# Kernel tuning notes

Hardware: AMD Instinct MI355X
Metric: run time of the kernel (lower is better)

## Reference

```python
import jax, jax.numpy as jnp
import numpy as np
from functools import partial

DN = ('NCHW', 'OIHW', 'NCHW')

def _conv(x, w, b, stride, pad):
    y = jax.lax.conv_general_dilated(x, w, (stride, stride), [(pad, pad), (pad, pad)], dimension_numbers=DN)
    return y + b[None, :, None, None]

def _leaky(x, s):
    return jnp.where(x >= 0, x, s * x)

def _lstm_gates(pre, c):
    # PyTorch gate order: i, f, g, o
    i, f, g, o = jnp.split(pre, 4, axis=-1)
    c_new = jax.nn.sigmoid(f) * c + jax.nn.sigmoid(i) * jnp.tanh(g)
    h_new = jax.nn.sigmoid(o) * jnp.tanh(c_new)
    return h_new, c_new

def setup_inputs() -> dict:
    key = jax.random.key(0)
    ks = iter(jax.random.split(key, 32))
    s = 0.05
    d = {}
    d['x'] = jax.random.normal(next(ks), (128, 3, 64, 64), jnp.float32)
    # conv stack params
    d['w1'] = jax.random.normal(next(ks), (64, 3, 7, 7)) * s;   d['b1'] = jnp.zeros((64,))
    d['w2'] = jax.random.normal(next(ks), (128, 64, 7, 7)) * s; d['b2'] = jnp.zeros((128,))
    d['w3'] = jax.random.normal(next(ks), (256, 128, 5, 5)) * s; d['b3'] = jnp.zeros((256,))
    d['w4'] = jax.random.normal(next(ks), (512, 256, 5, 5)) * s; d['b4'] = jnp.zeros((512,))
    d['w5'] = jax.random.normal(next(ks), (512, 512, 5, 5)) * s; d['b5'] = jnp.zeros((512,))
    # 2-layer LSTM (hidden=512), PyTorch layout: W_ih [4H, In], W_hh [4H, H]
    H = 512
    for l in range(2):
        d[f'wih{l}'] = jax.random.normal(next(ks), (4 * H, H)) * s
        d[f'whh{l}'] = jax.random.normal(next(ks), (4 * H, H)) * s
        d[f'bih{l}'] = jnp.zeros((4 * H,))
        d[f'bhh{l}'] = jnp.zeros((4 * H,))
    # FC head
    d['fw1'] = jax.random.normal(next(ks), (512, 512)) * s; d['fb1'] = jnp.zeros((512,))
    d['fw2'] = jax.random.normal(next(ks), (13, 512)) * s;  d['fb2'] = jnp.zeros((13,))
    return d

TIMESTEPS = 20

def reference(x, w1, b1, w2, b2, w3, b3, w4, b4, w5, b5,
              wih0, whh0, bih0, bhh0, wih1, whh1, bih1, bhh1,
              fw1, fb1, fw2, fb2):
    B = x.shape[0]
    h = _conv(x, w1, b1, 2, 3); h = _leaky(h, 0.2)
    h = _conv(h, w2, b2, 2, 0); h = _leaky(h, 0.2)
    h = _conv(h, w3, b3, 1, 0); h = _leaky(h, 0.2)
    h = _conv(h, w4, b4, 1, 0); h = _leaky(h, 0.2)
    h = _conv(h, w5, b5, 1, 0); h = _leaky(h, 0.2)
    feat = h.reshape(B, -1)  # [B, 512]
    H = 512
    # input to layer-0 is constant across timesteps: precompute Wx once
    xW0 = feat @ wih0.T + bih0 + bhh0  # [B, 4H]
    zeros = jnp.zeros((B, H), feat.dtype)

    def step(carry, _):
        h0, c0, h1, c1 = carry
        h0n, c0n = _lstm_gates(xW0 + h0 @ whh0.T, c0)
        pre1 = h0n @ wih1.T + bih1 + bhh1 + h1 @ whh1.T
        h1n, c1n = _lstm_gates(pre1, c1)
        return (h0n, c0n, h1n, c1n), h1n

    _, ys = jax.lax.scan(step, (zeros, zeros, zeros, zeros), None, length=TIMESTEPS)
    y = ys.reshape(TIMESTEPS * B, H)
    y = _leaky(y @ fw1.T + fb1, 0.01)
    y = jax.nn.sigmoid(y @ fw2.T + fb2)
    return y
```

## Files before the change

kernel.cpp:

```cpp
#include <hip/hip_runtime.h>
#include <math.h>

typedef _Float16 half_t;
typedef __attribute__((ext_vector_type(8))) _Float16 f16x8;
typedef __attribute__((ext_vector_type(4))) _Float16 f16x4;
typedef __attribute__((ext_vector_type(4))) float f32x4;

#define LEAKY(v, s) ((v) >= 0.f ? (v) : (s) * (v))

__device__ __forceinline__ float sig_(float x) { return 1.f / (1.f + expf(-x)); }
__device__ __forceinline__ half_t f2h(float f) { return (half_t)f; }

#define GLD(gp, lp)                                              \
  __builtin_amdgcn_global_load_lds(                              \
      (const __attribute__((address_space(1))) void*)(gp),       \
      (__attribute__((address_space(3))) void*)(lp), 16, 0, 0)

#define PHASE_WAIT(N)                                            \
  asm volatile("s_waitcnt vmcnt(" #N ")" ::: "memory");          \
  __builtin_amdgcn_s_barrier();                                  \
  __builtin_amdgcn_sched_barrier(0)

#define QOFF0 2048LL
#define QOFF1 4096LL
#define QOFF2 135168LL
#define QOFF3 266240LL
#define QOFF4 5283840LL
#define QOFF5 5310464LL
#define QOFF6 6359040LL
#define QOFF7 6621184LL
#define QOFF8 7669760LL
#define QOFF9 9766912LL

__global__ void prep_all(
    const float* __restrict__ x, const float* __restrict__ w1,
    const float* __restrict__ wih0, const float* __restrict__ whh0,
    const float* __restrict__ bih0, const float* __restrict__ bhh0,
    const float* __restrict__ wih1, const float* __restrict__ whh1,
    const float* __restrict__ bih1, const float* __restrict__ bhh1,
    const float* __restrict__ fw1,
    float* __restrict__ bg0, float* __restrict__ bg1,
    float* __restrict__ czero, unsigned* __restrict__ hzero,
    half_t* __restrict__ xpad, half_t* __restrict__ w1r,
    half_t* __restrict__ wih0h, half_t* __restrict__ fw1h,
    half_t* __restrict__ wcat0h, half_t* __restrict__ wcat1h) {
  long long i = (long long)blockIdx.x * blockDim.x + threadIdx.x;
  if (i < QOFF0) {
    bg0[i] = bih0[i] + bhh0[i];
  } else if (i < QOFF1) {
    long long j = i - QOFF0;
    bg1[j] = bih1[j] + bhh1[j];
  } else if (i < QOFF2) {
    czero[i - QOFF1] = 0.f;
  } else if (i < QOFF3) {
    hzero[i - QOFF2] = 0u;
  } else if (i < QOFF4) {
    long long j = i - QOFF3;
    int c = j & 7;
    long long t = j >> 3;
    int iw = t % 70; t /= 70;
    int ih = t % 70;
    int n = t / 70;
    float v = 0.f;
    if (c < 3 && ih >= 3 && ih < 67 && iw >= 3 && iw < 67)
      v = x[((n * 3 + c) * 64 + (ih - 3)) * 64 + (iw - 3)];
    xpad[j] = f2h(v);
  } else if (i < QOFF5) {
    int j = (int)(i - QOFF4);
    int kg = j % 416, co = j / 416;
    int ci = kg & 7, tap = kg >> 3;
    float v = 0.f;
    if (tap < 49 && ci < 3) {
      int kh = tap / 7, kw = tap % 7;
      v = w1[((co * 3 + ci) * 7 + kh) * 7 + kw];
    }
    w1r[j] = f2h(v);
  } else if (i < QOFF6) {
    int j = (int)(i - QOFF5);
    wih0h[j] = f2h(wih0[j]);
  } else if (i < QOFF7) {
    int j = (int)(i - QOFF6);
    fw1h[j] = f2h(fw1[j]);
  } else if (i < QOFF8) {
    int j = (int)(i - QOFF7);
    int r = j >> 9, k = j & 511;
    int u = r >> 2, g = r & 3;
    wcat0h[j] = f2h(whh0[(g * 512 + u) * 512 + k]);
  } else if (i < QOFF9) {
    int j = (int)(i - QOFF8);
    int r = j >> 10, k = j & 1023;
    int u = r >> 2, g = r & 3;
    int row = g * 512 + u;
    wcat1h[j] = f2h(k < 512 ? wih1[row * 512 + k] : whh1[row * 512 + (k - 512)]);
  }
}

__global__ __launch_bounds__(256) void prep_wT(
    const float* __restrict__ w2, const float* __restrict__ w3,
    const float* __restrict__ w4, const float* __restrict__ w5,
    half_t* __restrict__ w2r, half_t* __restrict__ w3r,
    half_t* __restrict__ w4r, half_t* __restrict__ w5r) {
  __shared__ float T[12800];
  int bid = blockIdx.x, tid = threadIdx.x;
  const float* W;
  half_t* D;
  int co, Cin, TAP, lg2;
  if (bid < 128) {
    W = w2; D = w2r; co = bid; Cin = 64; TAP = 49; lg2 = 6;
  } else if (bid < 384) {
    W = w3; D = w3r; co = bid - 128; Cin = 128; TAP = 25; lg2 = 7;
  } else if (bid < 896) {
    W = w4; D = w4r; co = bid - 384; Cin = 256; TAP = 25; lg2 = 8;
  } else {
    W = w5; D = w5r; co = bid - 896; Cin = 512; TAP = 25; lg2 = 9;
  }
  int n = Cin * TAP;
  const float* src = W + (size_t)co * n;
  for (int i = tid; i < n; i += 256) T[i] = src[i];
  __syncthreads();
  half_t* dst = D + (size_t)co * n;
  for (int j = tid; j < n; j += 256) {
    int ci = j & (Cin - 1);
    int tap = j >> lg2;
    dst[j] = f2h(T[ci * TAP + tap]);
  }
}

template <int KW, int S, int LOG2CIN, int OUTMODE>
__global__ __launch_bounds__(256) void conv_mfma(
    const half_t* __restrict__ xin, const half_t* __restrict__ wr,
    const float* __restrict__ bias, void* __restrict__ outp,
    int Hin, int Win, int Hout, int Wout, int Cout, int K, int ktiles, float slope,
    long long zstride) {
  constexpr int CIN = 1 << LOG2CIN;
  __shared__ half_t lds[4][4096];
  const int tid = threadIdx.x;
  const int lane = tid & 63, wid = tid >> 6;
  const int sRow = tid >> 2, sCh = tid & 3;
  const int sSwz = sCh ^ ((sRow ^ (sRow >> 2)) & 3);
  const int kt0 = blockIdx.z * ktiles;
  const half_t* gArow = wr + (size_t)(blockIdx.y * 64 + sRow) * K + sSwz * 8;
  int p = blockIdx.x * 64 + sRow;
  int hw = Hout * Wout;
  int n = p / hw;
  int rem = p - n * hw;
  int oh = rem / Wout;
  int ow = rem - oh * Wout;
  const half_t* xb = xin + ((size_t)(n * Hin + oh * S) * Win + ow * S) * CIN;
  const int fr = lane & 15, fc = lane >> 4;
  const int r0 = (wid & 1) * 32, c0 = (wid >> 1) * 32;
  const int sw = (fc ^ ((fr ^ (fr >> 2)) & 3)) * 8;
  const int ia0 = (r0 + fr) * 32 + sw;
  const int ia1 = (r0 + 16 + fr) * 32 + sw;
  const int ib0 = 2048 + (c0 + fr) * 32 + sw;
  const int ib1 = 2048 + (c0 + 16 + fr) * 32 + sw;

  auto stage = [&](int t, int buf) {
    GLD(gArow + (size_t)(kt0 + t) * 32, &lds[buf][wid * 512]);
    int kg = (kt0 + t) * 32 + sSwz * 8;
    int ci = kg & (CIN - 1);
    int tap = kg >> LOG2CIN;
    int kh = tap / KW, kw = tap - kh * KW;
    GLD(xb + (kh * Win + kw) * CIN + ci, &lds[buf][2048 + wid * 512]);
  };

  f32x4 acc00 = {0.f, 0.f, 0.f, 0.f};
  f32x4 acc01 = acc00, acc10 = acc00, acc11 = acc00;

  auto compute = [&](int buf) {
    const half_t* L = &lds[buf][0];
    f16x8 a0 = *(const f16x8*)&L[ia0];
    f16x8 a1 = *(const f16x8*)&L[ia1];
    f16x8 b0 = *(const f16x8*)&L[ib0];
    f16x8 b1 = *(const f16x8*)&L[ib1];
    acc00 = __builtin_amdgcn_mfma_f32_16x16x32_f16(a0, b0, acc00, 0, 0, 0);
    acc01 = __builtin_amdgcn_mfma_f32_16x16x32_f16(a0, b1, acc01, 0, 0, 0);
    acc10 = __builtin_amdgcn_mfma_f32_16x16x32_f16(a1, b0, acc10, 0, 0, 0);
    acc11 = __builtin_amdgcn_mfma_f32_16x16x32_f16(a1, b1, acc11, 0, 0, 0);
  };

  stage(0, 0);
  stage(1, 1);
  stage(2, 2);
  int t = 0;
  for (; t < ktiles - 3; ++t) {
    PHASE_WAIT(4);
    stage(t + 3, (t + 3) & 3);
    compute(t & 3);
  }
  PHASE_WAIT(4);
  compute(t & 3);
  ++t;
  PHASE_WAIT(2);
  compute(t & 3);
  ++t;
  PHASE_WAIT(0);
  compute(t & 3);

#pragma unroll
  for (int am = 0; am < 2; ++am) {
#pragma unroll
    for (int bn = 0; bn < 2; ++bn) {
      f32x4 a = am == 0 ? (bn == 0 ? acc00 : acc01) : (bn == 0 ? acc10 : acc11);
      int co = blockIdx.y * 64 + r0 + am * 16 + fc * 4;
      int px = blockIdx.x * 64 + c0 + bn * 16 + fr;
      size_t o = (size_t)px * Cout + co;
      if (OUTMODE == 2) {
        float* pb = (float*)outp + (size_t)blockIdx.z * zstride;
        *(f32x4*)&pb[o] = a;
      } else {
        f32x4 bb = *(const f32x4*)&bias[co];
        f32x4 v;
#pragma unroll
        for (int j = 0; j < 4; ++j) {
          float tt = a[j] + bb[j];
          v[j] = LEAKY(tt, slope);
        }
        if (OUTMODE == 1) {
          *(f32x4*)&((float*)outp)[o] = v;
        } else {
          f16x4 hv;
#pragma unroll
          for (int j = 0; j < 4; ++j) hv[j] = f2h(v[j]);
          *(f16x4*)&((half_t*)outp)[o] = hv;
        }
      }
    }
  }
}

template <int KW, int S, int LOG2CIN, int OUTMODE>
__global__ __launch_bounds__(256) void conv_mfma128(
    const half_t* __restrict__ xin, const half_t* __restrict__ wr,
    const float* __restrict__ bias, void* __restrict__ outp,
    int Hin, int Win, int Hout, int Wout, int Cout, int K, int ktiles, float slope,
    long long zstride, int Y, int G) {
  constexpr int CIN = 1 << LOG2CIN;
  __shared__ half_t lds[4][8192];
  const int L = blockIdx.x;
  const int bx = L / G;
  const int g = L % G;
  const int by = g % Y;
  const int bz = g / Y;
  const int tid = threadIdx.x;
  const int lane = tid & 63, wid = tid >> 6;
  const int sRow = tid >> 2, sCh = tid & 3;
  const int sSwz = sCh ^ ((sRow ^ (sRow >> 2)) & 3);
  const int kt0 = bz * ktiles;
  const half_t* gA0 = wr + (size_t)(by * 128 + sRow) * K + sSwz * 8;
  const half_t* gA1 = wr + (size_t)(by * 128 + 64 + sRow) * K + sSwz * 8;
  int hw = Hout * Wout;
  int p0 = bx * 128 + sRow;
  int n0 = p0 / hw, r0p = p0 - n0 * hw, oh0 = r0p / Wout, ow0 = r0p - oh0 * Wout;
  const half_t* xb0 = xin + ((size_t)(n0 * Hin + oh0 * S) * Win + ow0 * S) * CIN;
  int p1 = p0 + 64;
  int n1 = p1 / hw, r1p = p1 - n1 * hw, oh1 = r1p / Wout, ow1 = r1p - oh1 * Wout;
  const half_t* xb1 = xin + ((size_t)(n1 * Hin + oh1 * S) * Win + ow1 * S) * CIN;

  const int fr = lane & 15, fc = lane >> 4;
  const int wr_ = wid & 1, wc_ = wid >> 1;
  const int sw = (fc ^ ((fr ^ (fr >> 2)) & 3)) * 8;
  const int iaB = (wr_ * 64 + fr) * 32 + sw;
  const int ibB = 4096 + (wc_ * 64 + fr) * 32 + sw;

  auto stage = [&](int t, int buf) {
    half_t* LB = &lds[buf][0];
    GLD(gA0 + (size_t)(kt0 + t) * 32, LB + wid * 512);
    GLD(gA1 + (size_t)(kt0 + t) * 32, LB + 2048 + wid * 512);
    int kg = (kt0 + t) * 32 + sSwz * 8;
    int ci = kg & (CIN - 1);
    int tap = kg >> LOG2CIN;
    int kh = tap / KW, kw = tap - kh * KW;
    int xoff = (kh * Win + kw) * CIN + ci;
    GLD(xb0 + xoff, LB + 4096 + wid * 512);
    GLD(xb1 + xoff, LB + 6144 + wid * 512);
  };

  f32x4 acc[4][4];
#pragma unroll
  for (int i = 0; i < 4; ++i)
#pragma unroll
    for (int j = 0; j < 4; ++j) acc[i][j] = (f32x4){0.f, 0.f, 0.f, 0.f};

  auto compute = [&](int buf) {
    const half_t* L2 = &lds[buf][0];
    f16x8 a[4], b[4];
#pragma unroll
    for (int fi = 0; fi < 4; ++fi) a[fi] = *(const f16x8*)&L2[iaB + fi * 512];
#pragma unroll
    for (int fj = 0; fj < 4; ++fj) b[fj] = *(const f16x8*)&L2[ibB + fj * 512];
#pragma unroll
    for (int fi = 0; fi < 4; ++fi)
#pragma unroll
      for (int fj = 0; fj < 4; ++fj)
        acc[fi][fj] = __builtin_amdgcn_mfma_f32_16x16x32_f16(a[fi], b[fj], acc[fi][fj], 0, 0, 0);
  };

  stage(0, 0);
  stage(1, 1);
  stage(2, 2);
  int t = 0;
  for (; t < ktiles - 3; ++t) {
    PHASE_WAIT(8);
    stage(t + 3, (t + 3) & 3);
    compute(t & 3);
  }
  PHASE_WAIT(8);
  compute(t & 3);
  ++t;
  PHASE_WAIT(4);
  compute(t & 3);
  ++t;
  PHASE_WAIT(0);
  compute(t & 3);

#pragma unroll
  for (int fi = 0; fi < 4; ++fi) {
#pragma unroll
    for (int fj = 0; fj < 4; ++fj) {
      int co = by * 128 + wr_ * 64 + fi * 16 + fc * 4;
      int px = bx * 128 + wc_ * 64 + fj * 16 + fr;
      size_t o = (size_t)px * Cout + co;
      if (OUTMODE == 3) {
        half_t* pb = (half_t*)outp + (size_t)bz * zstride;
        f16x4 hv;
#pragma unroll
        for (int j = 0; j < 4; ++j) hv[j] = f2h(acc[fi][fj][j]);
        *(f16x4*)&pb[o] = hv;
      } else {
        f32x4 bb = *(const f32x4*)&bias[co];
        f16x4 hv;
#pragma unroll
        for (int j = 0; j < 4; ++j) {
          float tt = acc[fi][fj][j] + bb[j];
          hv[j] = f2h(LEAKY(tt, slope));
        }
        *(f16x4*)&((half_t*)outp)[o] = hv;
      }
    }
  }
}

__global__ void finalize_part(const float* __restrict__ pb, const float* __restrict__ bias,
                              half_t* __restrict__ out, int size, int nz) {
  int i = blockIdx.x * blockDim.x + threadIdx.x;
  if (i >= size) return;
  float s = bias[i & 511];
  for (int z = 0; z < nz; ++z) s += pb[(size_t)z * size + i];
  out[i] = f2h(LEAKY(s, 0.2f));
}

__global__ void finalize_h(const half_t* __restrict__ pb, const float* __restrict__ bias,
                           half_t* __restrict__ out, int size8, int nz, int cmask,
                           long long zstride) {
  int idx = blockIdx.x * blockDim.x + threadIdx.x;
  if (idx >= size8) return;
  long long i = (long long)idx * 8;
  float s[8];
#pragma unroll
  for (int q = 0; q < 8; ++q) s[q] = bias[(int)((i + q) & cmask)];
  for (int z = 0; z < nz; ++z) {
    f16x8 v = *(const f16x8*)&pb[(size_t)z * zstride + i];
#pragma unroll
    for (int q = 0; q < 8; ++q) s[q] += (float)v[q];
  }
  f16x8 o;
#pragma unroll
  for (int q = 0; q < 8; ++q) o[q] = f2h(LEAKY(s[q], 0.2f));
  *(f16x8*)&out[i] = o;
}

__global__ __launch_bounds__(256) void lstm_fused(
    const half_t* __restrict__ h0in, half_t* __restrict__ h0out,
    const half_t* __restrict__ h1in, half_t* __restrict__ h1out,
    const half_t* __restrict__ wcat0, const half_t* __restrict__ wcat1,
    const float* __restrict__ xw0, const float* __restrict__ bg1,
    float* __restrict__ c0, float* __restrict__ c1,
    half_t* __restrict__ ysout, int roles) {
  const bool isL1 = (roles == 2) || (blockIdx.z == 1);
  const int NT = isL1 ? 16 : 8;
  const half_t* wcat = isL1 ? wcat1 : wcat0;
  float* c = isL1 ? c1 : c0;
  half_t* hout = isL1 ? h1out : h0out;
  const int K = NT * 64;

  __shared__ half_t lds[4][8192];
  const int tid = threadIdx.x;
  const int lane = tid & 63, wid = tid >> 6;
  const int ybase = blockIdx.y * 64, bbase = blockIdx.x * 64;
  const int rA0 = wid * 16 + (lane >> 3);
  const int rA1 = rA0 + 8;
  const int chS = ((lane & 7) ^ ((lane >> 3) & 7)) * 8;
  const half_t* gA0 = wcat + (size_t)(ybase + rA0) * K + chS;
  const half_t* gA1 = wcat + (size_t)(ybase + rA1) * K + chS;
  const size_t hb0 = (size_t)(bbase + rA0) * 512 + chS;
  const size_t hb1 = (size_t)(bbase + rA1) * 512 + chS;

  auto stage = [&](int t, int buf) {
    GLD(gA0 + t * 64, &lds[buf][wid * 1024]);
    GLD(gA1 + t * 64, &lds[buf][wid * 1024 + 512]);
    const half_t* hs = (isL1 && t >= 8) ? h1in : h0in;
    int koff = (isL1 && t >= 8) ? (t - 8) * 64 : t * 64;
    GLD(hs + hb0 + koff, &lds[buf][4096 + wid * 1024]);
    GLD(hs + hb1 + koff, &lds[buf][4096 + wid * 1024 + 512]);
  };

  const int fr = lane & 15, fc = lane >> 4;
  const int wr_ = wid & 1, wc_ = wid >> 1;

  f32x4 acc[2][2];
#pragma unroll
  for (int fi = 0; fi < 2; ++fi)
#pragma unroll
    for (int fj = 0; fj < 2; ++fj) acc[fi][fj] = (f32x4){0.f, 0.f, 0.f, 0.f};

  auto compute = [&](int buf) {
    const half_t* L = &lds[buf][0];
#pragma unroll
    for (int s = 0; s < 2; ++s) {
      f16x8 a[2], b[2];
#pragma unroll
      for (int fi = 0; fi < 2; ++fi) {
        int row = wr_ * 32 + fi * 16 + fr;
        a[fi] = *(const f16x8*)&L[row * 64 + (((s * 4 + fc) ^ (fr & 7)) * 8)];
      }
#pragma unroll
      for (int fj = 0; fj < 2; ++fj) {
        int brow = wc_ * 32 + fj * 16 + fr;
        b[fj] = *(const f16x8*)&L[4096 + brow * 64 + (((s * 4 + fc) ^ (fr & 7)) * 8)];
      }
#pragma unroll
      for (int fi = 0; fi < 2; ++fi)
#pragma unroll
        for (int fj = 0; fj < 2; ++fj)
          acc[fi][fj] = __builtin_amdgcn_mfma_f32_16x16x32_f16(a[fi], b[fj], acc[fi][fj], 0, 0, 0);
    }
  };

  stage(0, 0);
  stage(1, 1);
  stage(2, 2);
  int t = 0;
  for (; t < NT - 3; ++t) {
    PHASE_WAIT(8);
    stage(t + 3, (t + 3) & 3);
    compute(t & 3);
  }
  PHASE_WAIT(8);
  compute(t & 3);
  ++t;
  PHASE_WAIT(4);
  compute(t & 3);
  ++t;
  PHASE_WAIT(0);
  compute(t & 3);

#pragma unroll
  for (int fi = 0; fi < 2; ++fi) {
#pragma unroll
    for (int fj = 0; fj < 2; ++fj) {
      int Rb = ybase + wr_ * 32 + fi * 16 + fc * 4;
      int u = Rb >> 2;
      int b = bbase + wc_ * 32 + fj * 16 + fr;
      float p[4];
#pragma unroll
      for (int j = 0; j < 4; ++j) {
        float s = acc[fi][fj][j];
        s += isL1 ? bg1[j * 512 + u] : xw0[b * 2048 + j * 512 + u];
        p[j] = s;
      }
      int ci = b * 512 + u;
      float cprev = c[ci];
      float ig = sig_(p[0]);
      float fg = sig_(p[1]);
      float gg = tanhf(p[2]);
      float og = sig_(p[3]);
      float cn = fg * cprev + ig * gg;
      float hn = og * tanhf(cn);
      c[ci] = cn;
      hout[ci] = f2h(hn);
      if (isL1) ysout[ci] = f2h(hn);
    }
  }
}

__global__ void fc2_sigmoid(const half_t* __restrict__ in, const float* __restrict__ w,
                            const float* __restrict__ b, float* __restrict__ out) {
  int idx = blockIdx.x * blockDim.x + threadIdx.x;
  if (idx >= 2560 * 13) return;
  int j = idx % 13, r = idx / 13;
  const half_t* ip = in + (size_t)r * 512;
  const float* wp = w + j * 512;
  float s = b[j];
  for (int k = 0; k < 512; k += 8) {
    f16x8 hv = *(const f16x8*)&ip[k];
#pragma unroll
    for (int q = 0; q < 8; ++q) s = fmaf((float)hv[q], wp[k + q], s);
  }
  out[idx] = sig_(s);
}

extern "C" void kernel_launch(void* const* d_in, const int* in_sizes, int n_in,
                              void* d_out, int out_size, void* d_ws, size_t ws_size,
                              hipStream_t stream) {
  const float* x   = (const float*)d_in[0];
  const float* w1  = (const float*)d_in[1];  const float* b1 = (const float*)d_in[2];
  const float* w2  = (const float*)d_in[3];  const float* b2 = (const float*)d_in[4];
  const float* w3  = (const float*)d_in[5];  const float* b3 = (const float*)d_in[6];
  const float* w4  = (const float*)d_in[7];  const float* b4 = (const float*)d_in[8];
  const float* w5  = (const float*)d_in[9];  const float* b5 = (const float*)d_in[10];
  const float* wih0 = (const float*)d_in[11]; const float* whh0 = (const float*)d_in[12];
  const float* bih0 = (const float*)d_in[13]; const float* bhh0 = (const float*)d_in[14];
  const float* wih1 = (const float*)d_in[15]; const float* whh1 = (const float*)d_in[16];
  const float* bih1 = (const float*)d_in[17]; const float* bhh1 = (const float*)d_in[18];
  const float* fw1 = (const float*)d_in[19]; const float* fb1 = (const float*)d_in[20];
  const float* fw2 = (const float*)d_in[21]; const float* fb2 = (const float*)d_in[22];
  float* out = (float*)d_out;

  float* bg0 = (float*)d_ws;
  float* bg1 = bg0 + 2048;
  float* xw0 = bg1 + 2048;
  float* c0  = xw0 + 262144;
  float* c1  = c0 + 65536;
  half_t* h0a = (half_t*)(c1 + 65536);
  half_t* h0b = h0a + 65536;
  half_t* h1a = h0b + 65536;
  half_t* h1b = h1a + 65536;
  half_t* BUF1 = h1b + 65536;
  half_t* BUF2 = BUF1 + 8388608;
  half_t* w1r  = BUF2 + 2768896;
  half_t* w2r  = w1r + 26624;
  half_t* w3r  = w2r + 401408;
  half_t* w4r  = w3r + 819200;
  half_t* w5r  = w4r + 3276800;
  half_t* wih0h  = w5r + 6553600;
  half_t* wcat0h = wih0h + 1048576;
  half_t* wcat1h = wcat0h + 1048576;
  half_t* fw1h   = wcat1h + 2097152;
  half_t* xpad   = fw1h + 262144;
  half_t* pbH = xpad;
  float* pbC = (float*)xpad;

  half_t* A1 = BUF1;
  half_t* A2 = BUF2;
  half_t* A3 = BUF1;
  half_t* A4 = BUF2;
  half_t* feat = BUF1;
  half_t* ys   = BUF2;
  half_t* fc1o = BUF2 + 1310720;

  dim3 blk(256);

  prep_all<<<38152, blk, 0, stream>>>(
      x, w1, wih0, whh0, bih0, bhh0, wih1, whh1, bih1, bhh1, fw1,
      bg0, bg1, c0, (unsigned*)h0a, xpad, w1r, wih0h, fw1h, wcat0h, wcat1h);
  prep_wT<<<1408, blk, 0, stream>>>(w2, w3, w4, w5, w2r, w3r, w4r, w5r);

  conv_mfma<7, 2, 3, 0><<<dim3(2048, 1, 1), blk, 0, stream>>>(
      xpad, w1r, b1, A1, 70, 70, 32, 32, 64, 416, 13, 0.2f, 0);
  conv_mfma128<7, 2, 6, 3><<<338, blk, 0, stream>>>(
      A1, w2r, b2, pbH, 32, 32, 13, 13, 128, 3136, 49, 0.2f, 2768896LL, 1, 2);
  finalize_h<<<1352, blk, 0, stream>>>(pbH, b2, A2, 346112, 2, 127, 2768896LL);
  conv_mfma128<5, 1, 7, 3><<<324, blk, 0, stream>>>(
      A2, w3r, b3, pbH, 13, 13, 9, 9, 256, 3200, 50, 0.2f, 2654208LL, 2, 4);
  finalize_h<<<1296, blk, 0, stream>>>(pbH, b3, A3, 331776, 2, 255, 2654208LL);
  conv_mfma128<5, 1, 8, 3><<<400, blk, 0, stream>>>(
      A3, w4r, b4, pbH, 9, 9, 5, 5, 512, 6400, 50, 0.2f, 1638400LL, 4, 16);
  finalize_h<<<800, blk, 0, stream>>>(pbH, b4, A4, 204800, 4, 511, 1638400LL);
  conv_mfma<5, 1, 9, 2><<<dim3(2, 8, 25), blk, 0, stream>>>(
      A4, w5r, b5, pbC, 5, 5, 1, 1, 512, 12800, 16, 0.2f, (long long)65536);
  finalize_part<<<256, blk, 0, stream>>>(pbC, b5, feat, 65536, 25);

  conv_mfma<1, 1, 9, 1><<<dim3(2, 32, 1), blk, 0, stream>>>(
      feat, wih0h, bg0, xw0, 1, 1, 1, 1, 2048, 512, 16, 1.0f, 0);

  half_t* h0buf[2] = {h0a, h0b};
  half_t* h1buf[2] = {h1a, h1b};
  lstm_fused<<<dim3(2, 32, 1), blk, 0, stream>>>(
      h0a, h0b, h1a, h1a, wcat0h, wcat1h, xw0, bg1, c0, c1, ys, 1);
  for (int t = 2; t <= 20; ++t) {
    lstm_fused<<<dim3(2, 32, 2), blk, 0, stream>>>(
        h0buf[(t - 1) & 1], h0buf[t & 1], h1buf[t & 1], h1buf[(t - 1) & 1],
        wcat0h, wcat1h, xw0, bg1, c0, c1, ys + (size_t)(t - 2) * 65536, 3);
  }
  lstm_fused<<<dim3(2, 32, 1), blk, 0, stream>>>(
      h0buf[0], h0buf[1], h1buf[1], h1buf[0],
      wcat0h, wcat1h, xw0, bg1, c0, c1, ys + (size_t)19 * 65536, 2);

  conv_mfma<1, 1, 9, 0><<<dim3(40, 8, 1), blk, 0, stream>>>(
      ys, fw1h, fb1, fc1o, 1, 1, 1, 1, 512, 512, 16, 0.01f, 0);
  fc2_sigmoid<<<130, blk, 0, stream>>>(fc1o, fw2, fb2, out);
}
```

Baseline: 399.7 us.

## Overlap FC1 slices with LSTM steps and raise MFMA wave priority

The FC1 (fw1) GEMM over each finished timestep's hidden output is folded into the next LSTM step launch as an extra grid z-slice, so FC1 work fills idle CUs during the latency-bound recurrent steps. Only the last timestep's FC1 runs in a small standalone launch afterward. Separately, s_setprio is raised around the MFMA blocks in the conv and LSTM kernels to favour waves issuing matrix ops. This adds role dispatch and more kernel arguments, and the epilogue layout of the FC path must match the old conv output.

```diff
diff --git a/kernel.cpp b/kernel.cpp
--- a/kernel.cpp
+++ b/kernel.cpp
@@ -173,10 +173,12 @@
     f16x8 a1 = *(const f16x8*)&L[ia1];
     f16x8 b0 = *(const f16x8*)&L[ib0];
     f16x8 b1 = *(const f16x8*)&L[ib1];
+    __builtin_amdgcn_s_setprio(1);
     acc00 = __builtin_amdgcn_mfma_f32_16x16x32_f16(a0, b0, acc00, 0, 0, 0);
     acc01 = __builtin_amdgcn_mfma_f32_16x16x32_f16(a0, b1, acc01, 0, 0, 0);
     acc10 = __builtin_amdgcn_mfma_f32_16x16x32_f16(a1, b0, acc10, 0, 0, 0);
     acc11 = __builtin_amdgcn_mfma_f32_16x16x32_f16(a1, b1, acc11, 0, 0, 0);
+    __builtin_amdgcn_s_setprio(0);
   };
 
   stage(0, 0);
@@ -289,11 +291,13 @@
     for (int fi = 0; fi < 4; ++fi) a[fi] = *(const f16x8*)&L2[iaB + fi * 512];
 #pragma unroll
     for (int fj = 0; fj < 4; ++fj) b[fj] = *(const f16x8*)&L2[ibB + fj * 512];
+    __builtin_amdgcn_s_setprio(1);
 #pragma unroll
     for (int fi = 0; fi < 4; ++fi)
 #pragma unroll
       for (int fj = 0; fj < 4; ++fj)
         acc[fi][fj] = __builtin_amdgcn_mfma_f32_16x16x32_f16(a[fi], b[fj], acc[fi][fj], 0, 0, 0);
+    __builtin_amdgcn_s_setprio(0);
   };
 
   stage(0, 0);
@@ -376,12 +380,15 @@
     const half_t* __restrict__ wcat0, const half_t* __restrict__ wcat1,
     const float* __restrict__ xw0, const float* __restrict__ bg1,
     float* __restrict__ c0, float* __restrict__ c1,
-    half_t* __restrict__ ysout, int roles) {
-  const bool isL1 = (roles == 2) || (blockIdx.z == 1);
+    half_t* __restrict__ ysout, int zl1, int zfc,
+    const half_t* __restrict__ fcw, const float* __restrict__ fcb,
+    const half_t* __restrict__ fcin, half_t* __restrict__ fcout) {
+  const int bzp = blockIdx.z;
+  const bool isFC = (bzp == zfc);
+  const bool isL1 = (bzp == zl1);
+  if (isFC && blockIdx.y >= 8) return;
   const int NT = isL1 ? 16 : 8;
-  const half_t* wcat = isL1 ? wcat1 : wcat0;
-  float* c = isL1 ? c1 : c0;
-  half_t* hout = isL1 ? h1out : h0out;
+  const half_t* Asrc = isFC ? fcw : (isL1 ? wcat1 : wcat0);
   const int K = NT * 64;
 
   __shared__ half_t lds[4][8192];
@@ -391,15 +398,16 @@
   const int rA0 = wid * 16 + (lane >> 3);
   const int rA1 = rA0 + 8;
   const int chS = ((lane & 7) ^ ((lane >> 3) & 7)) * 8;
-  const half_t* gA0 = wcat + (size_t)(ybase + rA0) * K + chS;
-  const half_t* gA1 = wcat + (size_t)(ybase + rA1) * K + chS;
+  const half_t* gA0 = Asrc + (size_t)(ybase + rA0) * K + chS;
+  const half_t* gA1 = Asrc + (size_t)(ybase + rA1) * K + chS;
   const size_t hb0 = (size_t)(bbase + rA0) * 512 + chS;
   const size_t hb1 = (size_t)(bbase + rA1) * 512 + chS;
+  const half_t* bsrc0 = isFC ? fcin : h0in;
 
   auto stage = [&](int t, int buf) {
     GLD(gA0 + t * 64, &lds[buf][wid * 1024]);
     GLD(gA1 + t * 64, &lds[buf][wid * 1024 + 512]);
-    const half_t* hs = (isL1 && t >= 8) ? h1in : h0in;
+    const half_t* hs = (isL1 && t >= 8) ? h1in : bsrc0;
     int koff = (isL1 && t >= 8) ? (t - 8) * 64 : t * 64;
     GLD(hs + hb0 + koff, &lds[buf][4096 + wid * 1024]);
     GLD(hs + hb1 + koff, &lds[buf][4096 + wid * 1024 + 512]);
@@ -429,11 +437,13 @@
         int brow = wc_ * 32 + fj * 16 + fr;
         b[fj] = *(const f16x8*)&L[4096 + brow * 64 + (((s * 4 + fc) ^ (fr & 7)) * 8)];
       }
+      __builtin_amdgcn_s_setprio(1);
 #pragma unroll
       for (int fi = 0; fi < 2; ++fi)
 #pragma unroll
         for (int fj = 0; fj < 2; ++fj)
           acc[fi][fj] = __builtin_amdgcn_mfma_f32_16x16x32_f16(a[fi], b[fj], acc[fi][fj], 0, 0, 0);
+      __builtin_amdgcn_s_setprio(0);
     }
   };
 
@@ -455,6 +465,28 @@
   PHASE_WAIT(0);
   compute(t & 3);
 
+  if (isFC) {
+#pragma unroll
+    for (int fi = 0; fi < 2; ++fi) {
+#pragma unroll
+      for (int fj = 0; fj < 2; ++fj) {
+        int Rb = ybase + wr_ * 32 + fi * 16 + fc * 4;
+        int b = bbase + wc_ * 32 + fj * 16 + fr;
+        f32x4 bb = *(const f32x4*)&fcb[Rb];
+        f16x4 hv;
+#pragma unroll
+        for (int j = 0; j < 4; ++j) {
+          float tt = acc[fi][fj][j] + bb[j];
+          hv[j] = f2h(LEAKY(tt, 0.01f));
+        }
+        *(f16x4*)&fcout[(size_t)b * 512 + Rb] = hv;
+      }
+    }
+    return;
+  }
+
+  float* c = isL1 ? c1 : c0;
+  half_t* hout = isL1 ? h1out : h0out;
 #pragma unroll
   for (int fi = 0; fi < 2; ++fi) {
 #pragma unroll
@@ -577,17 +609,24 @@
   half_t* h0buf[2] = {h0a, h0b};
   half_t* h1buf[2] = {h1a, h1b};
   lstm_fused<<<dim3(2, 32, 1), blk, 0, stream>>>(
-      h0a, h0b, h1a, h1a, wcat0h, wcat1h, xw0, bg1, c0, c1, ys, 1);
-  for (int t = 2; t <= 20; ++t) {
-    lstm_fused<<<dim3(2, 32, 2), blk, 0, stream>>>(
+      h0a, h0b, h1a, h1a, wcat0h, wcat1h, xw0, bg1, c0, c1, ys,
+      -1, -1, fw1h, fb1, nullptr, nullptr);
+  lstm_fused<<<dim3(2, 32, 2), blk, 0, stream>>>(
+      h0buf[1], h0buf[0], h1buf[0], h1buf[1], wcat0h, wcat1h, xw0, bg1, c0, c1,
+      ys, 1, -1, fw1h, fb1, nullptr, nullptr);
+  for (int t = 3; t <= 20; ++t) {
+    lstm_fused<<<dim3(2, 32, 3), blk, 0, stream>>>(
         h0buf[(t - 1) & 1], h0buf[t & 1], h1buf[t & 1], h1buf[(t - 1) & 1],
-        wcat0h, wcat1h, xw0, bg1, c0, c1, ys + (size_t)(t - 2) * 65536, 3);
-  }
-  lstm_fused<<<dim3(2, 32, 1), blk, 0, stream>>>(
+        wcat0h, wcat1h, xw0, bg1, c0, c1, ys + (size_t)(t - 2) * 65536,
+        1, 2, fw1h, fb1, ys + (size_t)(t - 3) * 65536, fc1o + (size_t)(t - 3) * 65536);
+  }
+  lstm_fused<<<dim3(2, 32, 2), blk, 0, stream>>>(
       h0buf[0], h0buf[1], h1buf[1], h1buf[0],
-      wcat0h, wcat1h, xw0, bg1, c0, c1, ys + (size_t)19 * 65536, 2);
-
-  conv_mfma<1, 1, 9, 0><<<dim3(40, 8, 1), blk, 0, stream>>>(
-      ys, fw1h, fb1, fc1o, 1, 1, 1, 1, 512, 512, 16, 0.01f, 0);
+      wcat0h, wcat1h, xw0, bg1, c0, c1, ys + (size_t)19 * 65536,
+      0, 1, fw1h, fb1, ys + (size_t)18 * 65536, fc1o + (size_t)18 * 65536);
+
+  conv_mfma<1, 1, 9, 0><<<dim3(2, 8, 1), blk, 0, stream>>>(
+      ys + (size_t)19 * 65536, fw1h, fb1, fc1o + (size_t)19 * 65536,
+      1, 1, 1, 1, 512, 512, 16, 0.01f, 0);
   fc2_sigmoid<<<130, blk, 0, stream>>>(fc1o, fw2, fb2, out);
 }
```

Measured after the change: 410.0 us. 2.6% more time.
